# Kernel optimization log

Measured on AMD Instinct MI355X. Metric: run time of the kernel, lower is better.

Reference implementation:

```python
import jax, jax.numpy as jnp
import numpy as np
from jax import lax

B, H, W = 16, 256, 256
NUM_HIDDEN = 12
C = 3 + NUM_HIDDEN + 1  # 16 channels: rgb + hidden + alpha
HID = 64
ALPHA = 1.0
THR = 0.1

SOBEL_X = jnp.array([[-1.0, 0.0, 1.0], [-2.0, 0.0, 2.0], [-1.0, 0.0, 1.0]], jnp.float32) / 8.0
SOBEL_Y = jnp.array([[-1.0, -2.0, -1.0], [0.0, 0.0, 0.0], [1.0, 2.0, 1.0]], jnp.float32) / 8.0


def _sobel_conv(s, k):
    # s: [B,H,W] channel-summed state; k: [3,3]. SAME-padded 2D stencil.
    return lax.conv_general_dilated(
        s[..., None], k[:, :, None, None], window_strides=(1, 1), padding='SAME',
        dimension_numbers=('NHWC', 'HWIO', 'NHWC'))  # [B,H,W,1]


def _alive(x, thr):
    # 3x3 max-pool over alpha channel (index 3), SAME padding.
    a = x[..., 3:4]
    pooled = lax.reduce_window(a, -jnp.inf, lax.max, (1, 3, 3, 1), (1, 1, 1, 1), 'SAME')
    return pooled > thr  # [B,H,W,1] bool


def setup_inputs() -> dict:
    key = jax.random.key(0)
    ks = jax.random.split(key, 7)
    x = jax.random.uniform(ks[0], (B, H, W, C), dtype=jnp.float32)
    # UpdateNet params: 1x1 convs stored as dense matrices [in, out].
    w1 = jax.random.normal(ks[1], (3 * C, HID), dtype=jnp.float32) * (1.0 / np.sqrt(3 * C))
    b1 = jnp.zeros((HID,), jnp.float32)
    w2 = jax.random.normal(ks[2], (HID, HID), dtype=jnp.float32) * (1.0 / np.sqrt(HID))
    b2 = jnp.zeros((HID,), jnp.float32)
    # Original zero-inits w3; use small random values so outputs/grads are nontrivial.
    w3 = jax.random.normal(ks[3], (HID, C), dtype=jnp.float32) * 0.01
    return {'x': x, 'w1': w1, 'b1': b1, 'w2': w2, 'b2': b2, 'w3': w3}


def reference(x, w1, b1, w2, b2, w3):
    pre_life = _alive(x, THR)
    # Sobel perception: kernel[o,i] = sobel for all o,i  =>  each output channel
    # is the sobel filter applied to the channel-sum; broadcast across C channels.
    s = jnp.sum(x, axis=-1)                      # [B,H,W]
    sx = _sobel_conv(s, SOBEL_X)                 # [B,H,W,1]
    sy = _sobel_conv(s, SOBEL_Y)                 # [B,H,W,1]
    perc = jnp.concatenate(
        [x, jnp.broadcast_to(sx, x.shape), jnp.broadcast_to(sy, x.shape)], axis=-1)  # [B,H,W,3C]
    # UpdateNet: two biased 1x1 convs + ReLU, then unbiased 1x1 conv.
    h = jax.nn.relu(jnp.einsum('bhwi,io->bhwo', perc, w1) + b1)
    h = jax.nn.relu(jnp.einsum('bhwi,io->bhwo', h, w2) + b2)
    update = jnp.einsum('bhwi,io->bhwo', h, w3)  # [B,H,W,C]
    # cell_fire_rate == 1.0 -> stochastic update mask is all ones.
    x_new = x + ALPHA * update
    post_life = _alive(x_new, THR)
    life = (pre_life & post_life).astype(x_new.dtype)
    return x_new * life
```

## Files before the change

### kernel.cpp

```cpp
#include <hip/hip_runtime.h>
#include <hip/hip_bf16.h>
#include <cstdint>

#define NPIX (16 * 256 * 256)
#define THRV 0.1f

typedef __bf16 bf16x8 __attribute__((ext_vector_type(8)));
typedef float  f32x4  __attribute__((ext_vector_type(4)));

#define NSLOT 18

__global__ __launch_bounds__(256) void k_prep(const float* __restrict__ x,
                                              const float* __restrict__ w1,
                                              const float* __restrict__ b1,
                                              const float* __restrict__ w2,
                                              const float* __restrict__ b2,
                                              const float* __restrict__ w3,
                                              float2* __restrict__ hxs,
                                              unsigned char* __restrict__ rpre,
                                              float4* __restrict__ wpack) {
    __shared__ float sS[258];
    __shared__ float sA[258];
    const int tid = threadIdx.x;
    const int p = blockIdx.x * 256 + tid;

    const float4* xp = (const float4*)(x + (size_t)p * 16);
    float4 a = xp[0], b = xp[1], c = xp[2], d = xp[3];
    float sum = ((a.x + a.y) + (a.z + a.w)) + ((b.x + b.y) + (b.z + b.w)) +
                ((c.x + c.y) + (c.z + c.w)) + ((d.x + d.y) + (d.z + d.w));
    sS[tid + 1] = sum;
    sA[tid + 1] = a.w;
    if (tid == 0) { sS[0] = 0.f; sS[257] = 0.f; sA[0] = -1e30f; sA[257] = -1e30f; }
    __syncthreads();

    hxs[p] = make_float2(sS[tid + 2] - sS[tid],
                         sS[tid] + 2.f * sS[tid + 1] + sS[tid + 2]);
    float rm = fmaxf(sA[tid], fmaxf(sA[tid + 1], sA[tid + 2]));
    rpre[p] = (rm > THRV) ? 1 : 0;

    if (blockIdx.x == 0 && tid < 64) {
        const int lane = tid;
        const int r = lane & 15, g = lane >> 4;
#pragma unroll
        for (int n = 0; n < 4; ++n) {
            const int cc = n * 16 + r;
            bf16x8 f;
#pragma unroll
            for (int j = 0; j < 8; ++j) {
                float v = 0.f;
                if (j < 4) v = w1[(g * 4 + j) * 64 + cc];
                else if (g == 0 && j == 4) { for (int t = 0; t < 16; ++t) v += w1[(16 + t) * 64 + cc]; }
                else if (g == 0 && j == 5) { for (int t = 0; t < 16; ++t) v += w1[(32 + t) * 64 + cc]; }
                else if (g == 1 && j == 4) v = b1[cc];
                f[j] = (__bf16)v;
            }
            wpack[n * 64 + lane] = *(const float4*)&f;
        }
#pragma unroll
        for (int s = 0; s < 2; ++s)
#pragma unroll
            for (int n = 0; n < 4; ++n) {
                bf16x8 f;
#pragma unroll
                for (int j = 0; j < 8; ++j) {
                    const int psi = (2 * s + (j >> 2)) * 16 + g * 4 + (j & 3);
                    f[j] = (__bf16)w2[psi * 64 + n * 16 + r];
                }
                wpack[(4 + s * 4 + n) * 64 + lane] = *(const float4*)&f;
            }
#pragma unroll
        for (int s = 0; s < 2; ++s) {
            bf16x8 f;
#pragma unroll
            for (int j = 0; j < 8; ++j) {
                const int psi = (2 * s + (j >> 2)) * 16 + g * 4 + (j & 3);
                f[j] = (__bf16)w3[psi * 16 + r];
            }
            wpack[(12 + s) * 64 + lane] = *(const float4*)&f;
        }
#pragma unroll
        for (int n = 0; n < 4; ++n) {
            f32x4 v;
#pragma unroll
            for (int q = 0; q < 4; ++q) v[q] = b2[n * 16 + g * 4 + q];
            wpack[(14 + n) * 64 + lane] = *(const float4*)&v;
        }
    }
}

__global__ __launch_bounds__(256) void k_mfma(const float* __restrict__ x,
                                              const float2* __restrict__ hxs,
                                              const float4* __restrict__ wpack,
                                              float* __restrict__ out,
                                              unsigned char* __restrict__ anewf) {
    const int tid = threadIdx.x;
    const int wv = tid >> 6, lane = tid & 63;
    const int r = lane & 15, g = lane >> 4;

    bf16x8 w1f[4], w2f[2][4], w3f[2];
    f32x4 b2v[4];
#pragma unroll
    for (int n = 0; n < 4; ++n) { float4 t = wpack[n * 64 + lane]; w1f[n] = *(bf16x8*)&t; }
#pragma unroll
    for (int s2 = 0; s2 < 2; ++s2)
#pragma unroll
        for (int n = 0; n < 4; ++n) { float4 t = wpack[(4 + s2 * 4 + n) * 64 + lane]; w2f[s2][n] = *(bf16x8*)&t; }
#pragma unroll
    for (int s2 = 0; s2 < 2; ++s2) { float4 t = wpack[(12 + s2) * 64 + lane]; w3f[s2] = *(bf16x8*)&t; }
#pragma unroll
    for (int n = 0; n < 4; ++n) { float4 t = wpack[(14 + n) * 64 + lane]; b2v[n] = *(f32x4*)&t; }

    const int row = (blockIdx.x & 7) * 512 + (blockIdx.x >> 3);
    const int y = row & 255;
    const size_t rbase = (size_t)row * 256;
    const int wcol = wv * 64;
    const float2* hrow = hxs + rbase;
    const bool ymok = (y > 0), ypok = (y < 255);

    float4 xf[4];
    float2 h0[4], h1[4], h2[4];
#pragma unroll
    for (int t = 0; t < 4; ++t) {
        const int col = wcol + t * 16 + r;
        xf[t] = *(const float4*)(x + (rbase + col) * 16 + g * 4);
        h0[t] = ymok ? hrow[col - 256] : make_float2(0.f, 0.f);
        h1[t] = hrow[col];
        h2[t] = ypok ? hrow[col + 256] : make_float2(0.f, 0.f);
    }

#pragma unroll
    for (int t = 0; t < 4; ++t) {
        const int col = wcol + t * 16 + r;
        const size_t pix = rbase + col;

        const float gx = (h0[t].x + 2.f * h1[t].x + h2[t].x) * 0.125f;
        const float gy = (h2[t].y - h0[t].y) * 0.125f;

        bf16x8 a1;
        a1[0] = (__bf16)xf[t].x; a1[1] = (__bf16)xf[t].y;
        a1[2] = (__bf16)xf[t].z; a1[3] = (__bf16)xf[t].w;
        a1[4] = (__bf16)(g == 0 ? gx : (g == 1 ? 1.f : 0.f));
        a1[5] = (__bf16)(g == 0 ? gy : 0.f);
        a1[6] = (__bf16)0.f; a1[7] = (__bf16)0.f;

        f32x4 acc1[4];
#pragma unroll
        for (int n = 0; n < 4; ++n)
            acc1[n] = __builtin_amdgcn_mfma_f32_16x16x32_bf16(
                w1f[n], a1, (f32x4){0.f, 0.f, 0.f, 0.f}, 0, 0, 0);

        bf16x8 bf2[2];
#pragma unroll
        for (int s2 = 0; s2 < 2; ++s2)
#pragma unroll
            for (int j = 0; j < 4; ++j) {
                bf2[s2][j]     = (__bf16)fmaxf(acc1[2 * s2][j], 0.f);
                bf2[s2][4 + j] = (__bf16)fmaxf(acc1[2 * s2 + 1][j], 0.f);
            }

        f32x4 acc2[4];
#pragma unroll
        for (int n = 0; n < 4; ++n) {
            acc2[n] = b2v[n];
            acc2[n] = __builtin_amdgcn_mfma_f32_16x16x32_bf16(w2f[0][n], bf2[0], acc2[n], 0, 0, 0);
            acc2[n] = __builtin_amdgcn_mfma_f32_16x16x32_bf16(w2f[1][n], bf2[1], acc2[n], 0, 0, 0);
        }

        bf16x8 bf3[2];
#pragma unroll
        for (int s2 = 0; s2 < 2; ++s2)
#pragma unroll
            for (int j = 0; j < 4; ++j) {
                bf3[s2][j]     = (__bf16)fmaxf(acc2[2 * s2][j], 0.f);
                bf3[s2][4 + j] = (__bf16)fmaxf(acc2[2 * s2 + 1][j], 0.f);
            }

        f32x4 acc3 = __builtin_amdgcn_mfma_f32_16x16x32_bf16(
            w3f[0], bf3[0], (f32x4){0.f, 0.f, 0.f, 0.f}, 0, 0, 0);
        acc3 = __builtin_amdgcn_mfma_f32_16x16x32_bf16(w3f[1], bf3[1], acc3, 0, 0, 0);

        f32x4 xn;
        xn[0] = xf[t].x + acc3[0]; xn[1] = xf[t].y + acc3[1];
        xn[2] = xf[t].z + acc3[2]; xn[3] = xf[t].w + acc3[3];
        __builtin_nontemporal_store(xn, (f32x4*)(out + pix * 16 + g * 4));
        if (g == 0) anewf[pix] = (xn[3] > THRV) ? 1 : 0;
    }
}

__global__ __launch_bounds__(256) void k_post(const unsigned char* __restrict__ rpre,
                                              const unsigned char* __restrict__ anewf,
                                              float* __restrict__ out) {
    const int q = blockIdx.x * 256 + threadIdx.x;
    const int p0 = q * 4;
    const int bi = p0 >> 16;
    const int rem = p0 & 65535;
    const int y = rem >> 8;
    const int c0 = rem & 255;
    const unsigned char* pr = rpre + ((size_t)bi << 16);
    const unsigned char* an = anewf + ((size_t)bi << 16);

    unsigned pre = 0, M = 0, l = 0, rr = 0;
#pragma unroll
    for (int dy = -1; dy <= 1; ++dy) {
        const int y2 = y + dy;
        if ((unsigned)y2 >= 256u) continue;
        const int ro = y2 * 256;
        pre |= *(const unsigned*)(pr + ro + c0);
        M   |= *(const unsigned*)(an + ro + c0);
        l   |= (c0 > 0)   ? (unsigned)an[ro + c0 - 1] : 0u;
        rr  |= (c0 < 252) ? (unsigned)an[ro + c0 + 4] : 0u;
    }
    const unsigned post = M | (M << 8) | l | (M >> 8) | (rr << 24);
    const unsigned alive = pre & post;
    if (alive != 0x01010101u) {
        const f32x4 z = (f32x4){0.f, 0.f, 0.f, 0.f};
#pragma unroll
        for (int i = 0; i < 4; ++i)
            if (!((alive >> (8 * i)) & 1u)) {
                f32x4* op = (f32x4*)(out + (size_t)(p0 + i) * 16);
                op[0] = z; op[1] = z; op[2] = z; op[3] = z;
            }
    }
}

extern "C" void kernel_launch(void* const* d_in, const int* in_sizes, int n_in,
                              void* d_out, int out_size, void* d_ws, size_t ws_size,
                              hipStream_t stream) {
    const float* x  = (const float*)d_in[0];
    const float* w1 = (const float*)d_in[1];
    const float* b1 = (const float*)d_in[2];
    const float* w2 = (const float*)d_in[3];
    const float* b2 = (const float*)d_in[4];
    const float* w3 = (const float*)d_in[5];
    float* out = (float*)d_out;

    float2* hxs = (float2*)d_ws;
    unsigned char* rpre  = (unsigned char*)(hxs + NPIX);
    unsigned char* anewf = rpre + NPIX;
    float4* wpack = (float4*)(anewf + NPIX);

    hipLaunchKernelGGL(k_prep, dim3(NPIX / 256), dim3(256), 0, stream,
                       x, w1, b1, w2, b2, w3, hxs, rpre, wpack);
    hipLaunchKernelGGL(k_mfma, dim3(NPIX / 256), dim3(256), 0, stream,
                       x, hxs, wpack, out, anewf);
    hipLaunchKernelGGL(k_post, dim3(NPIX / 1024), dim3(256), 0, stream,
                       rpre, anewf, out);
}
```

Before: 50.46 us.

## Fuse Sobel and pre-life computation into MFMA kernel, split weight packing

Removes the full-grid prep kernel that wrote per-pixel horizontal Sobel partials and pre-alive flags, and computes the channel sums and stencils inside the MLP kernel. Neighbor rows are read directly from x and combined through shared memory. A tiny single-block kernel now packs the weights. This cuts one full pass over x and the hxs intermediate round trip, but each block reads three rows of x (the row above and below are redundant reads, likely L2 hits) and adds a barrier before the MFMA work.

```diff
diff --git a/kernel.cpp b/kernel.cpp
--- a/kernel.cpp
+++ b/kernel.cpp
@@ -10,131 +10,147 @@
 
 #define NSLOT 18
 
-__global__ __launch_bounds__(256) void k_prep(const float* __restrict__ x,
-                                              const float* __restrict__ w1,
-                                              const float* __restrict__ b1,
-                                              const float* __restrict__ w2,
-                                              const float* __restrict__ b2,
-                                              const float* __restrict__ w3,
-                                              float2* __restrict__ hxs,
-                                              unsigned char* __restrict__ rpre,
-                                              float4* __restrict__ wpack) {
-    __shared__ float sS[258];
-    __shared__ float sA[258];
-    const int tid = threadIdx.x;
-    const int p = blockIdx.x * 256 + tid;
-
-    const float4* xp = (const float4*)(x + (size_t)p * 16);
-    float4 a = xp[0], b = xp[1], c = xp[2], d = xp[3];
-    float sum = ((a.x + a.y) + (a.z + a.w)) + ((b.x + b.y) + (b.z + b.w)) +
-                ((c.x + c.y) + (c.z + c.w)) + ((d.x + d.y) + (d.z + d.w));
-    sS[tid + 1] = sum;
-    sA[tid + 1] = a.w;
-    if (tid == 0) { sS[0] = 0.f; sS[257] = 0.f; sA[0] = -1e30f; sA[257] = -1e30f; }
-    __syncthreads();
-
-    hxs[p] = make_float2(sS[tid + 2] - sS[tid],
-                         sS[tid] + 2.f * sS[tid + 1] + sS[tid + 2]);
-    float rm = fmaxf(sA[tid], fmaxf(sA[tid + 1], sA[tid + 2]));
-    rpre[p] = (rm > THRV) ? 1 : 0;
-
-    if (blockIdx.x == 0 && tid < 64) {
-        const int lane = tid;
-        const int r = lane & 15, g = lane >> 4;
+__global__ __launch_bounds__(64) void k_pack(const float* __restrict__ w1,
+                                             const float* __restrict__ b1,
+                                             const float* __restrict__ w2,
+                                             const float* __restrict__ b2,
+                                             const float* __restrict__ w3,
+                                             float4* __restrict__ wpack) {
+    const int lane = threadIdx.x;
+    const int r = lane & 15, g = lane >> 4;
+#pragma unroll
+    for (int n = 0; n < 4; ++n) {
+        const int cc = n * 16 + r;
+        bf16x8 f;
+#pragma unroll
+        for (int j = 0; j < 8; ++j) {
+            float v = 0.f;
+            if (j < 4) v = w1[(g * 4 + j) * 64 + cc];
+            else if (g == 0 && j == 4) { for (int t = 0; t < 16; ++t) v += w1[(16 + t) * 64 + cc]; }
+            else if (g == 0 && j == 5) { for (int t = 0; t < 16; ++t) v += w1[(32 + t) * 64 + cc]; }
+            else if (g == 1 && j == 4) v = b1[cc];
+            f[j] = (__bf16)v;
+        }
+        wpack[n * 64 + lane] = *(const float4*)&f;
+    }
+#pragma unroll
+    for (int s = 0; s < 2; ++s)
 #pragma unroll
         for (int n = 0; n < 4; ++n) {
-            const int cc = n * 16 + r;
-            bf16x8 f;
-#pragma unroll
-            for (int j = 0; j < 8; ++j) {
-                float v = 0.f;
-                if (j < 4) v = w1[(g * 4 + j) * 64 + cc];
-                else if (g == 0 && j == 4) { for (int t = 0; t < 16; ++t) v += w1[(16 + t) * 64 + cc]; }
-                else if (g == 0 && j == 5) { for (int t = 0; t < 16; ++t) v += w1[(32 + t) * 64 + cc]; }
-                else if (g == 1 && j == 4) v = b1[cc];
-                f[j] = (__bf16)v;
-            }
-            wpack[n * 64 + lane] = *(const float4*)&f;
-        }
-#pragma unroll
-        for (int s = 0; s < 2; ++s)
-#pragma unroll
-            for (int n = 0; n < 4; ++n) {
-                bf16x8 f;
-#pragma unroll
-                for (int j = 0; j < 8; ++j) {
-                    const int psi = (2 * s + (j >> 2)) * 16 + g * 4 + (j & 3);
-                    f[j] = (__bf16)w2[psi * 64 + n * 16 + r];
-                }
-                wpack[(4 + s * 4 + n) * 64 + lane] = *(const float4*)&f;
-            }
-#pragma unroll
-        for (int s = 0; s < 2; ++s) {
             bf16x8 f;
 #pragma unroll
             for (int j = 0; j < 8; ++j) {
                 const int psi = (2 * s + (j >> 2)) * 16 + g * 4 + (j & 3);
-                f[j] = (__bf16)w3[psi * 16 + r];
-            }
-            wpack[(12 + s) * 64 + lane] = *(const float4*)&f;
-        }
-#pragma unroll
-        for (int n = 0; n < 4; ++n) {
-            f32x4 v;
-#pragma unroll
-            for (int q = 0; q < 4; ++q) v[q] = b2[n * 16 + g * 4 + q];
-            wpack[(14 + n) * 64 + lane] = *(const float4*)&v;
-        }
-    }
-}
-
-__global__ __launch_bounds__(256) void k_mfma(const float* __restrict__ x,
-                                              const float2* __restrict__ hxs,
-                                              const float4* __restrict__ wpack,
-                                              float* __restrict__ out,
-                                              unsigned char* __restrict__ anewf) {
+                f[j] = (__bf16)w2[psi * 64 + n * 16 + r];
+            }
+            wpack[(4 + s * 4 + n) * 64 + lane] = *(const float4*)&f;
+        }
+#pragma unroll
+    for (int s = 0; s < 2; ++s) {
+        bf16x8 f;
+#pragma unroll
+        for (int j = 0; j < 8; ++j) {
+            const int psi = (2 * s + (j >> 2)) * 16 + g * 4 + (j & 3);
+            f[j] = (__bf16)w3[psi * 16 + r];
+        }
+        wpack[(12 + s) * 64 + lane] = *(const float4*)&f;
+    }
+#pragma unroll
+    for (int n = 0; n < 4; ++n) {
+        f32x4 v;
+#pragma unroll
+        for (int q = 0; q < 4; ++q) v[q] = b2[n * 16 + g * 4 + q];
+        wpack[(14 + n) * 64 + lane] = *(const float4*)&v;
+    }
+}
+
+__global__ __launch_bounds__(256) void k_fused(const float* __restrict__ x,
+                                               const float4* __restrict__ wpack,
+                                               float* __restrict__ out,
+                                               unsigned char* __restrict__ rpre,
+                                               unsigned char* __restrict__ anewf) {
+    __shared__ float sH0[256], sC[256], sH2[256], sC3[256];
+
     const int tid = threadIdx.x;
     const int wv = tid >> 6, lane = tid & 63;
     const int r = lane & 15, g = lane >> 4;
-
-    bf16x8 w1f[4], w2f[2][4], w3f[2];
-    f32x4 b2v[4];
-#pragma unroll
-    for (int n = 0; n < 4; ++n) { float4 t = wpack[n * 64 + lane]; w1f[n] = *(bf16x8*)&t; }
-#pragma unroll
-    for (int s2 = 0; s2 < 2; ++s2)
-#pragma unroll
-        for (int n = 0; n < 4; ++n) { float4 t = wpack[(4 + s2 * 4 + n) * 64 + lane]; w2f[s2][n] = *(bf16x8*)&t; }
-#pragma unroll
-    for (int s2 = 0; s2 < 2; ++s2) { float4 t = wpack[(12 + s2) * 64 + lane]; w3f[s2] = *(bf16x8*)&t; }
-#pragma unroll
-    for (int n = 0; n < 4; ++n) { float4 t = wpack[(14 + n) * 64 + lane]; b2v[n] = *(f32x4*)&t; }
 
     const int row = (blockIdx.x & 7) * 512 + (blockIdx.x >> 3);
     const int y = row & 255;
     const size_t rbase = (size_t)row * 256;
     const int wcol = wv * 64;
-    const float2* hrow = hxs + rbase;
     const bool ymok = (y > 0), ypok = (y < 255);
 
+    float4 ha0 = {0,0,0,0}, ha1 = {0,0,0,0}, ha2 = {0,0,0,0}, ha3 = {0,0,0,0};
+    float4 hb0 = {0,0,0,0}, hb1 = {0,0,0,0}, hb2 = {0,0,0,0}, hb3 = {0,0,0,0};
+    if (ymok) {
+        const float4* pm = (const float4*)(x + (rbase - 256 + tid) * 16);
+        ha0 = pm[0]; ha1 = pm[1]; ha2 = pm[2]; ha3 = pm[3];
+    }
+    if (ypok) {
+        const float4* pp = (const float4*)(x + (rbase + 256 + tid) * 16);
+        hb0 = pp[0]; hb1 = pp[1]; hb2 = pp[2]; hb3 = pp[3];
+    }
     float4 xf[4];
-    float2 h0[4], h1[4], h2[4];
 #pragma unroll
     for (int t = 0; t < 4; ++t) {
         const int col = wcol + t * 16 + r;
         xf[t] = *(const float4*)(x + (rbase + col) * 16 + g * 4);
-        h0[t] = ymok ? hrow[col - 256] : make_float2(0.f, 0.f);
-        h1[t] = hrow[col];
-        h2[t] = ypok ? hrow[col + 256] : make_float2(0.f, 0.f);
-    }
+    }
+
+    const float s0 = ((ha0.x + ha0.y) + (ha0.z + ha0.w)) + ((ha1.x + ha1.y) + (ha1.z + ha1.w)) +
+                     ((ha2.x + ha2.y) + (ha2.z + ha2.w)) + ((ha3.x + ha3.y) + (ha3.z + ha3.w));
+    const float s2 = ((hb0.x + hb0.y) + (hb0.z + hb0.w)) + ((hb1.x + hb1.y) + (hb1.z + hb1.w)) +
+                     ((hb2.x + hb2.y) + (hb2.z + hb2.w)) + ((hb3.x + hb3.y) + (hb3.z + hb3.w));
+    sH0[tid] = s0;
+    sH2[tid] = s2;
+
+#pragma unroll
+    for (int t = 0; t < 4; ++t) {
+        const int col = wcol + t * 16 + r;
+        float p = (xf[t].x + xf[t].y) + (xf[t].z + xf[t].w);
+        p += __shfl_xor(p, 16);
+        p += __shfl_xor(p, 32);
+        if (g == 0) { sC[col] = p; sC3[col] = xf[t].w; }
+    }
+    __syncthreads();
+
+    bf16x8 w1f[4], w2f[2][4], w3f[2];
+    f32x4 b2v[4];
+#pragma unroll
+    for (int n = 0; n < 4; ++n) { float4 t = wpack[n * 64 + lane]; w1f[n] = *(bf16x8*)&t; }
+#pragma unroll
+    for (int s2i = 0; s2i < 2; ++s2i)
+#pragma unroll
+        for (int n = 0; n < 4; ++n) { float4 t = wpack[(4 + s2i * 4 + n) * 64 + lane]; w2f[s2i][n] = *(bf16x8*)&t; }
+#pragma unroll
+    for (int s2i = 0; s2i < 2; ++s2i) { float4 t = wpack[(12 + s2i) * 64 + lane]; w3f[s2i] = *(bf16x8*)&t; }
+#pragma unroll
+    for (int n = 0; n < 4; ++n) { float4 t = wpack[(14 + n) * 64 + lane]; b2v[n] = *(f32x4*)&t; }
 
 #pragma unroll
     for (int t = 0; t < 4; ++t) {
         const int col = wcol + t * 16 + r;
         const size_t pix = rbase + col;
-
-        const float gx = (h0[t].x + 2.f * h1[t].x + h2[t].x) * 0.125f;
-        const float gy = (h2[t].y - h0[t].y) * 0.125f;
+        const bool cl = (col > 0), cr = (col < 255);
+
+        const float r0m = cl ? sH0[col - 1] : 0.f;
+        const float r0c = sH0[col];
+        const float r0p = cr ? sH0[col + 1] : 0.f;
+        const float r1m = cl ? sC[col - 1] : 0.f;
+        const float r1p = cr ? sC[col + 1] : 0.f;
+        const float r2m = cl ? sH2[col - 1] : 0.f;
+        const float r2c = sH2[col];
+        const float r2p = cr ? sH2[col + 1] : 0.f;
+        const float gx = ((r0p - r0m) + 2.f * (r1p - r1m) + (r2p - r2m)) * 0.125f;
+        const float gy = ((r2m + 2.f * r2c + r2p) - (r0m + 2.f * r0c + r0p)) * 0.125f;
+
+        if (g == 0) {
+            const float c3m = cl ? sC3[col - 1] : 0.f;
+            const float c3c = sC3[col];
+            const float c3p = cr ? sC3[col + 1] : 0.f;
+            rpre[pix] = (fmaxf(c3m, fmaxf(c3c, c3p)) > THRV) ? 1 : 0;
+        }
 
         bf16x8 a1;
         a1[0] = (__bf16)xf[t].x; a1[1] = (__bf16)xf[t].y;
@@ -151,11 +167,11 @@
 
         bf16x8 bf2[2];
 #pragma unroll
-        for (int s2 = 0; s2 < 2; ++s2)
+        for (int s2i = 0; s2i < 2; ++s2i)
 #pragma unroll
             for (int j = 0; j < 4; ++j) {
-                bf2[s2][j]     = (__bf16)fmaxf(acc1[2 * s2][j], 0.f);
-                bf2[s2][4 + j] = (__bf16)fmaxf(acc1[2 * s2 + 1][j], 0.f);
+                bf2[s2i][j]     = (__bf16)fmaxf(acc1[2 * s2i][j], 0.f);
+                bf2[s2i][4 + j] = (__bf16)fmaxf(acc1[2 * s2i + 1][j], 0.f);
             }
 
         f32x4 acc2[4];
@@ -168,11 +184,11 @@
 
         bf16x8 bf3[2];
 #pragma unroll
-        for (int s2 = 0; s2 < 2; ++s2)
+        for (int s2i = 0; s2i < 2; ++s2i)
 #pragma unroll
             for (int j = 0; j < 4; ++j) {
-                bf3[s2][j]     = (__bf16)fmaxf(acc2[2 * s2][j], 0.f);
-                bf3[s2][4 + j] = (__bf16)fmaxf(acc2[2 * s2 + 1][j], 0.f);
+                bf3[s2i][j]     = (__bf16)fmaxf(acc2[2 * s2i][j], 0.f);
+                bf3[s2i][4 + j] = (__bf16)fmaxf(acc2[2 * s2i + 1][j], 0.f);
             }
 
         f32x4 acc3 = __builtin_amdgcn_mfma_f32_16x16x32_bf16(
@@ -234,15 +250,13 @@
     const float* w3 = (const float*)d_in[5];
     float* out = (float*)d_out;
 
-    float2* hxs = (float2*)d_ws;
-    unsigned char* rpre  = (unsigned char*)(hxs + NPIX);
+    unsigned char* rpre  = (unsigned char*)d_ws;
     unsigned char* anewf = rpre + NPIX;
     float4* wpack = (float4*)(anewf + NPIX);
 
-    hipLaunchKernelGGL(k_prep, dim3(NPIX / 256), dim3(256), 0, stream,
-                       x, w1, b1, w2, b2, w3, hxs, rpre, wpack);
-    hipLaunchKernelGGL(k_mfma, dim3(NPIX / 256), dim3(256), 0, stream,
-                       x, hxs, wpack, out, anewf);
+    hipLaunchKernelGGL(k_pack, dim3(1), dim3(64), 0, stream, w1, b1, w2, b2, w3, wpack);
+    hipLaunchKernelGGL(k_fused, dim3(NPIX / 256), dim3(256), 0, stream,
+                       x, wpack, out, rpre, anewf);
     hipLaunchKernelGGL(k_post, dim3(NPIX / 1024), dim3(256), 0, stream,
                        rpre, anewf, out);
 }
```

Result: faster. 48.74 us (-3.4%).
